# Kernel tuning notes

Measured on AMD Instinct MI355X. Metric: run time of the kernel, lower is better.

Reference implementation:

```python
import jax, jax.numpy as jnp
import numpy as np

N_NODES = 150000
N_EDGES = 2400000
N_GRAPHS = 1024
EPS = 1e-5


def setup_inputs() -> dict:
    key = jax.random.key(0)
    ks = jax.random.split(key, 20)
    x = jax.random.normal(ks[0], (N_NODES, 3), dtype=jnp.float32)
    edge_index = jax.random.randint(ks[1], (2, N_EDGES), 0, N_NODES, dtype=jnp.int64)
    batch = jnp.sort(jax.random.randint(ks[2], (N_NODES,), 0, N_GRAPHS, dtype=jnp.int64))

    def glorot(k, shape):
        fan_in, fan_out = shape[0], shape[1]
        lim = jnp.sqrt(6.0 / (fan_in + fan_out)).astype(jnp.float32)
        return jax.random.uniform(k, shape, jnp.float32, -lim, lim)

    params = dict(
        W1=glorot(ks[3], (3, 32)), b1=jnp.zeros((32,), jnp.float32),
        gn1_w=jnp.ones((32,), jnp.float32), gn1_b=jnp.zeros((32,), jnp.float32), gn1_ms=jnp.ones((32,), jnp.float32),
        W2=glorot(ks[4], (32, 32)), b2=jnp.zeros((32,), jnp.float32),
        gn2_w=jnp.ones((32,), jnp.float32), gn2_b=jnp.zeros((32,), jnp.float32), gn2_ms=jnp.ones((32,), jnp.float32),
        W3=glorot(ks[5], (32, 32)), b3=jnp.zeros((32,), jnp.float32),
        gn3_w=jnp.ones((32,), jnp.float32), gn3_b=jnp.zeros((32,), jnp.float32), gn3_ms=jnp.ones((32,), jnp.float32),
        lin_w=glorot(ks[6], (32, 3)), lin_b=jnp.zeros((3,), jnp.float32),
    )
    return dict(x=x, edge_index=edge_index, batch=batch, **params)


def _gcn_conv(x, W, b, src, dst, dinv_sqrt):
    # PyG GCNConv: h = x @ W; propagate with sym-normalized A + self-loops; + bias
    h = x @ W  # [N, F]
    coef = dinv_sqrt[src] * dinv_sqrt[dst]  # [E]
    msgs = h[src] * coef[:, None]  # [E, F]
    agg = jax.ops.segment_sum(msgs, dst, num_segments=N_NODES)
    agg = agg + (dinv_sqrt * dinv_sqrt)[:, None] * h  # self-loop term
    return agg + b


def _graph_norm(x, batch, counts, weight, bias, mean_scale):
    # PyG GraphNorm: per-graph mean/var with learnable mean_scale
    mean = jax.ops.segment_sum(x, batch, num_segments=N_GRAPHS) / counts[:, None]
    out = x - mean_scale * mean[batch]
    var = jax.ops.segment_sum(out * out, batch, num_segments=N_GRAPHS) / counts[:, None]
    std = jnp.sqrt(var + EPS)
    return weight * out / std[batch] + bias


def reference(x, edge_index, batch,
              W1, b1, gn1_w, gn1_b, gn1_ms,
              W2, b2, gn2_w, gn2_b, gn2_ms,
              W3, b3, gn3_w, gn3_b, gn3_ms,
              lin_w, lin_b):
    src, dst = edge_index[0], edge_index[1]
    # degree over A + I (edge weight 1)
    deg = jax.ops.segment_sum(jnp.ones((N_EDGES,), jnp.float32), dst, num_segments=N_NODES) + 1.0
    dinv_sqrt = jax.lax.rsqrt(deg)
    counts = jax.ops.segment_sum(jnp.ones((N_NODES,), jnp.float32), batch, num_segments=N_GRAPHS)

    x1 = jax.nn.relu(_graph_norm(_gcn_conv(x, W1, b1, src, dst, dinv_sqrt), batch, counts, gn1_w, gn1_b, gn1_ms))
    h2 = _graph_norm(_gcn_conv(x1, W2, b2, src, dst, dinv_sqrt), batch, counts, gn2_w, gn2_b, gn2_ms)
    x2 = jax.nn.relu(h2 + x1)
    h3 = _graph_norm(_gcn_conv(x2, W3, b3, src, dst, dinv_sqrt), batch, counts, gn3_w, gn3_b, gn3_ms)
    x3 = jax.nn.relu(h3 + x2)

    pooled = jax.ops.segment_sum(x3, batch, num_segments=N_GRAPHS) / counts[:, None]  # mean pool
    return pooled @ lin_w + lin_b  # [G, 3]
```

## Files before the change

kernel.cpp:

```cpp
#include <hip/hip_runtime.h>

#define N_NODES 150000
#define N_EDGES 2400000
#define N_GRAPHS 1024
#define F 32
#define EPSV 1e-5f

#define BS 256
#define NB ((N_NODES + BS - 1) / BS)
#define CAP 5120
#define EB 8192
#define NEB ((N_EDGES + EB - 1) / EB)
#define EPT (EB / 256)
#define KPT (CAP / 256)

__device__ __forceinline__ float bflo(unsigned int u) {
    union { unsigned int i; float f; } v; v.i = u << 16; return v.f;
}
__device__ __forceinline__ float bfhi(unsigned int u) {
    union { unsigned int i; float f; } v; v.i = u & 0xffff0000u; return v.f;
}
__device__ __forceinline__ unsigned int f2bf(float f) {
    union { float f; unsigned int i; } v; v.f = f;
    unsigned int r = v.i + 0x7fff + ((v.i >> 16) & 1);
    return r >> 16;
}

__global__ void k_init(const int* __restrict__ batch, int* __restrict__ bucketCur,
                       int* __restrict__ off, float* __restrict__ gstats) {
    int i = blockIdx.x * blockDim.x + threadIdx.x;
    if (i >= N_NODES) return;
    if (i < NB) bucketCur[i] = i * CAP;
    if (i < N_GRAPHS * 9) gstats[i] = 0.f;
    int b = batch[i];
    if (i == 0) {
        for (int g = 0; g <= b; ++g) off[g] = 0;
    } else {
        int pb = batch[i - 1];
        for (int g = pb + 1; g <= b; ++g) off[g] = i;
    }
    if (i == N_NODES - 1) {
        for (int g = b + 1; g <= N_GRAPHS; ++g) off[g] = N_NODES;
    }
}

__global__ __launch_bounds__(256) void k_bin(const int* __restrict__ src,
                                             const int* __restrict__ dst,
                                             int* __restrict__ bucketCur,
                                             unsigned int* __restrict__ binned) {
    __shared__ int h[NB];
    __shared__ int gb[NB];
    int t = threadIdx.x;
    for (int b = t; b < NB; b += 256) h[b] = 0;
    __syncthreads();
    int base = blockIdx.x * EB + t;
    unsigned int key[EPT];
    unsigned int pk[EPT];
#pragma unroll
    for (int k = 0; k < EPT; ++k) {
        int e = base + k * 256;
        if (e < N_EDGES) {
            int d = dst[e];
            int b = d >> 8;
            key[k] = ((unsigned int)(d & 255) << 18) | (unsigned int)src[e];
            unsigned int rk = (unsigned int)atomicAdd(&h[b], 1);
            pk[k] = (rk << 10) | (unsigned int)b;
        } else {
            pk[k] = 0xFFFFFFFFu;
        }
    }
    __syncthreads();
    for (int b = t; b < NB; b += 256) {
        int c = h[b];
        gb[b] = c ? atomicAdd(&bucketCur[b], c) : 0;
    }
    __syncthreads();
#pragma unroll
    for (int k = 0; k < EPT; ++k) {
        if (pk[k] != 0xFFFFFFFFu) {
            unsigned int b = pk[k] & 1023u;
            unsigned int rk = pk[k] >> 10;
            binned[gb[b] + rk] = key[k];
        }
    }
}

__global__ __launch_bounds__(256) void k_csr(const unsigned int* __restrict__ binned,
                                             const int* __restrict__ bucketCur,
                                             const float* __restrict__ x,
                                             unsigned int* __restrict__ rowptr,
                                             float* __restrict__ dinv,
                                             float* __restrict__ xs4,
                                             int* __restrict__ csr) {
    __shared__ int lcnt[256];
    __shared__ int lpre[256];
    __shared__ int sc[256];
    int b = blockIdx.x, t = threadIdx.x;
    int e0 = b * CAP;
    int e1 = bucketCur[b];
    lcnt[t] = 0;
    __syncthreads();
    unsigned int kc[KPT];
#pragma unroll
    for (int k = 0; k < KPT; ++k) {
        int e = e0 + t + k * 256;
        if (e < e1) {
            kc[k] = binned[e];
            atomicAdd(&lcnt[kc[k] >> 18], 1);
        }
    }
    __syncthreads();
    int v = lcnt[t];
    sc[t] = v;
    __syncthreads();
    for (int o = 1; o < 256; o <<= 1) {
        int x2 = (t >= o) ? sc[t - o] : 0;
        __syncthreads();
        sc[t] += x2;
        __syncthreads();
    }
    int excl = sc[t] - v;
    lpre[t] = excl;
    int gnode = b * BS + t;
    if (gnode < N_NODES) {
        rowptr[gnode] = ((unsigned int)(e0 + excl) << 8) | (unsigned int)min(v, 255);
        float dv = rsqrtf((float)v + 1.0f);
        dinv[gnode] = dv;
        float4 xv;
        xv.x = x[gnode * 3 + 0] * dv;
        xv.y = x[gnode * 3 + 1] * dv;
        xv.z = x[gnode * 3 + 2] * dv;
        xv.w = 0.f;
        ((float4*)xs4)[gnode] = xv;
    }
    lcnt[t] = 0;
    __syncthreads();
#pragma unroll
    for (int k = 0; k < KPT; ++k) {
        int e = e0 + t + k * 256;
        if (e < e1) {
            unsigned int key = kc[k];
            int ld = key >> 18;
            int pos = atomicAdd(&lcnt[ld], 1);
            csr[e0 + lpre[ld] + pos] = (int)(key & 0x3FFFFu);
        }
    }
}

__global__ __launch_bounds__(256) void k_gz(
        const float* __restrict__ xs4, const int* __restrict__ csr,
        const unsigned int* __restrict__ rowptr, const float* __restrict__ dinv,
        const int* __restrict__ batch,
        float* __restrict__ zs4, float* __restrict__ gstats) {
    __shared__ float st[8 * 12];
    __shared__ int gbase_s;
    int t = threadIdx.x;
    for (int i = t; i < 8 * 12; i += 256) st[i] = 0.f;
    if (t == 0) gbase_s = batch[blockIdx.x * 128];
    __syncthreads();

    int gid = blockIdx.x * 256 + t;
    int n = gid >> 1, h = gid & 1;
    float z0 = 0.f, z1 = 0.f, z2 = 0.f;
    if (n < N_NODES) {
        const float4* xv = (const float4*)xs4;
        unsigned int rp = rowptr[n];
        int st0 = (int)(rp >> 8);
        int len = (int)(rp & 255u);
        int half0 = (len + 1) >> 1;
        int e  = h ? (st0 + half0) : st0;
        int e1 = h ? (st0 + len)   : (st0 + half0);
        if (!h) {
            float4 sv = xv[n];
            z0 = sv.x; z1 = sv.y; z2 = sv.z;
        }
        for (; e + 3 < e1; e += 4) {
            int s0 = csr[e], s1 = csr[e + 1], s2 = csr[e + 2], s3 = csr[e + 3];
            float4 u0 = xv[s0], u1 = xv[s1], u2 = xv[s2], u3 = xv[s3];
            z0 += u0.x + u1.x + u2.x + u3.x;
            z1 += u0.y + u1.y + u2.y + u3.y;
            z2 += u0.z + u1.z + u2.z + u3.z;
        }
        for (; e < e1; ++e) {
            float4 u = xv[csr[e]];
            z0 += u.x; z1 += u.y; z2 += u.z;
        }
    }
    z0 += __shfl_down(z0, 1);
    z1 += __shfl_down(z1, 1);
    z2 += __shfl_down(z2, 1);
    if (h == 0 && n < N_NODES) {
        float dd = dinv[n];
        z0 *= dd; z1 *= dd; z2 *= dd;
        float4 zv; zv.x = z0; zv.y = z1; zv.z = z2; zv.w = 0.f;
        ((float4*)zs4)[n] = zv;
        int g = batch[n];
        int lg = g - gbase_s;
        if (lg < 8) {
            float* sp = &st[lg * 12];
            atomicAdd(&sp[0], z0);      atomicAdd(&sp[1], z1);
            atomicAdd(&sp[2], z2);      atomicAdd(&sp[3], z0 * z0);
            atomicAdd(&sp[4], z0 * z1); atomicAdd(&sp[5], z0 * z2);
            atomicAdd(&sp[6], z1 * z1); atomicAdd(&sp[7], z1 * z2);
            atomicAdd(&sp[8], z2 * z2);
        } else {
            float* gp = &gstats[g * 9];
            atomicAdd(&gp[0], z0);      atomicAdd(&gp[1], z1);
            atomicAdd(&gp[2], z2);      atomicAdd(&gp[3], z0 * z0);
            atomicAdd(&gp[4], z0 * z1); atomicAdd(&gp[5], z0 * z2);
            atomicAdd(&gp[6], z1 * z1); atomicAdd(&gp[7], z1 * z2);
            atomicAdd(&gp[8], z2 * z2);
        }
    }
    __syncthreads();
    if (t < 72) {
        int slot = t / 9, k = t % 9;
        int g = gbase_s + slot;
        float v = st[slot * 12 + k];
        if (g < N_GRAPHS && v != 0.f) atomicAdd(&gstats[g * 9 + k], v);
    }
}

__global__ __launch_bounds__(256) void k_prep(
        const float* __restrict__ gstats, const int* __restrict__ off,
        const float* __restrict__ W, const float* __restrict__ bias,
        const float* __restrict__ gw, const float* __restrict__ gms,
        float* __restrict__ mvA, float* __restrict__ scA) {
    int gid = blockIdx.x * 256 + threadIdx.x;
    if (gid >= N_GRAPHS * F) return;
    int g = gid >> 5, f = gid & 31;
    float rc = 1.0f / (float)(off[g + 1] - off[g]);
    const float* sp = &gstats[g * 9];
    float S0 = sp[0], S1 = sp[1], S2 = sp[2];
    float m00 = sp[3], m01 = sp[4], m02 = sp[5], m11 = sp[6], m12 = sp[7], m22 = sp[8];
    float w0 = W[0 * F + f], w1 = W[1 * F + f], w2 = W[2 * F + f];
    float b = bias[f];
    float sy = w0 * S0 + w1 * S1 + w2 * S2;
    float m = sy * rc + b;
    float q = w0 * w0 * m00 + w1 * w1 * m11 + w2 * w2 * m22
            + 2.f * (w0 * w1 * m01 + w0 * w2 * m02 + w1 * w2 * m12);
    float Ey2 = q * rc + 2.f * b * (sy * rc) + b * b;
    float mv = gms[f] * m;
    float var = Ey2 - 2.f * mv * m + mv * mv;
    mvA[gid] = mv;
    scA[gid] = gw[f] * rsqrtf(var + EPSV);
}

__global__ __launch_bounds__(256) void k_n1(
        const float* __restrict__ zs4, const int* __restrict__ batch,
        const float* __restrict__ dinv,
        const float* __restrict__ W, const float* __restrict__ bias,
        const float* __restrict__ gb,
        const float* __restrict__ mvA, const float* __restrict__ scA,
        unsigned short* __restrict__ xh, float* __restrict__ outp) {
    int gid = blockIdx.x * 256 + threadIdx.x;
    int n = gid >> 3, c = gid & 7;
    if (n >= N_NODES) return;
    float4 zv = ((const float4*)zs4)[n];
    float z0 = zv.x, z1 = zv.y, z2 = zv.z;
    int g = batch[n];
    float dd = dinv[n];
    float4 w0 = ((const float4*)(W + 0 * F))[c];
    float4 w1 = ((const float4*)(W + 1 * F))[c];
    float4 w2 = ((const float4*)(W + 2 * F))[c];
    float4 y  = ((const float4*)bias)[c];
    y.x += z0 * w0.x + z1 * w1.x + z2 * w2.x;
    y.y += z0 * w0.y + z1 * w1.y + z2 * w2.y;
    y.z += z0 * w0.z + z1 * w1.z + z2 * w2.z;
    y.w += z0 * w0.w + z1 * w1.w + z2 * w2.w;
    float4 mv = ((const float4*)mvA)[g * 8 + c];
    float4 sc = ((const float4*)scA)[g * 8 + c];
    float4 bb = ((const float4*)gb)[c];
    float4 o;
    o.x = fmaxf((y.x - mv.x) * sc.x + bb.x, 0.f);
    o.y = fmaxf((y.y - mv.y) * sc.y + bb.y, 0.f);
    o.z = fmaxf((y.z - mv.z) * sc.z + bb.z, 0.f);
    o.w = fmaxf((y.w - mv.w) * sc.w + bb.w, 0.f);
    ((float4*)outp)[n * 8 + c] = o;
    uint2 hp;
    hp.x = f2bf(o.x * dd) | (f2bf(o.y * dd) << 16);
    hp.y = f2bf(o.z * dd) | (f2bf(o.w * dd) << 16);
    ((uint2*)xh)[n * 8 + c] = hp;
}

__global__ __launch_bounds__(256) void k_gat32(
        const unsigned short* __restrict__ xh, const int* __restrict__ csr,
        const unsigned int* __restrict__ rowptr, const float* __restrict__ dinv,
        const float* __restrict__ W, const float* __restrict__ bias,
        float* __restrict__ y) {
    __shared__ float Ws[F * F];
    __shared__ float bs[F];
    __shared__ float Zs[64 * 36];
    int t = threadIdx.x;
    ((float4*)Ws)[t] = ((const float4*)W)[t];
    if (t < F) bs[t] = bias[t];
    __syncthreads();

    int gid = blockIdx.x * 256 + t;
    int n = gid >> 2, c = gid & 3, ln = t >> 2;
    bool act = (n < N_NODES);
    float acc[8];
    if (act) {
        const uint4* xr = (const uint4*)xh;
        uint4 us = xr[n * 4 + c];
        acc[0] = bflo(us.x); acc[1] = bfhi(us.x);
        acc[2] = bflo(us.y); acc[3] = bfhi(us.y);
        acc[4] = bflo(us.z); acc[5] = bfhi(us.z);
        acc[6] = bflo(us.w); acc[7] = bfhi(us.w);
        unsigned int rp = rowptr[n];
        int e = (int)(rp >> 8);
        int e1 = e + (int)(rp & 255u);
        for (; e + 3 < e1; e += 4) {
            int s0 = csr[e], s1 = csr[e + 1], s2 = csr[e + 2], s3 = csr[e + 3];
            uint4 u0 = xr[s0 * 4 + c];
            uint4 u1 = xr[s1 * 4 + c];
            uint4 u2 = xr[s2 * 4 + c];
            uint4 u3 = xr[s3 * 4 + c];
            acc[0] += bflo(u0.x); acc[1] += bfhi(u0.x);
            acc[2] += bflo(u0.y); acc[3] += bfhi(u0.y);
            acc[4] += bflo(u0.z); acc[5] += bfhi(u0.z);
            acc[6] += bflo(u0.w); acc[7] += bfhi(u0.w);
            acc[0] += bflo(u1.x); acc[1] += bfhi(u1.x);
            acc[2] += bflo(u1.y); acc[3] += bfhi(u1.y);
            acc[4] += bflo(u1.z); acc[5] += bfhi(u1.z);
            acc[6] += bflo(u1.w); acc[7] += bfhi(u1.w);
            acc[0] += bflo(u2.x); acc[1] += bfhi(u2.x);
            acc[2] += bflo(u2.y); acc[3] += bfhi(u2.y);
            acc[4] += bflo(u2.z); acc[5] += bfhi(u2.z);
            acc[6] += bflo(u2.w); acc[7] += bfhi(u2.w);
            acc[0] += bflo(u3.x); acc[1] += bfhi(u3.x);
            acc[2] += bflo(u3.y); acc[3] += bfhi(u3.y);
            acc[4] += bflo(u3.z); acc[5] += bfhi(u3.z);
            acc[6] += bflo(u3.w); acc[7] += bfhi(u3.w);
        }
        for (; e < e1; ++e) {
            int s0 = csr[e];
            uint4 u0 = xr[s0 * 4 + c];
            acc[0] += bflo(u0.x); acc[1] += bfhi(u0.x);
            acc[2] += bflo(u0.y); acc[3] += bfhi(u0.y);
            acc[4] += bflo(u0.z); acc[5] += bfhi(u0.z);
            acc[6] += bflo(u0.w); acc[7] += bfhi(u0.w);
        }
        float dd = dinv[n];
#pragma unroll
        for (int j = 0; j < 8; ++j) acc[j] *= dd;
    } else {
#pragma unroll
        for (int j = 0; j < 8; ++j) acc[j] = 0.f;
    }
    *(float4*)&Zs[ln * 36 + c * 8]     = *(float4*)&acc[0];
    *(float4*)&Zs[ln * 36 + c * 8 + 4] = *(float4*)&acc[4];
    __syncthreads();

    if (act) {
        const float* zrow = &Zs[ln * 36];
        float4 o0 = ((const float4*)bs)[c * 2];
        float4 o1 = ((const float4*)bs)[c * 2 + 1];
#pragma unroll
        for (int k = 0; k < F; ++k) {
            float zk = zrow[k];
            float4 w0 = ((const float4*)&Ws[k * F])[c * 2];
            float4 w1 = ((const float4*)&Ws[k * F])[c * 2 + 1];
            o0.x += zk * w0.x; o0.y += zk * w0.y; o0.z += zk * w0.z; o0.w += zk * w0.w;
            o1.x += zk * w1.x; o1.y += zk * w1.y; o1.z += zk * w1.z; o1.w += zk * w1.w;
        }
        ((float4*)y)[n * 8 + c * 2]     = o0;
        ((float4*)y)[n * 8 + c * 2 + 1] = o1;
    }
}

template <bool RES, bool WXH>
__global__ __launch_bounds__(256) void k_gn2(
        const float* agg, const float* res, const int* __restrict__ off,
        const float* __restrict__ gw, const float* __restrict__ gb,
        const float* __restrict__ gms, const float* __restrict__ dinv,
        unsigned short* __restrict__ xh, float* outp) {
    __shared__ float red1[256], red2[256];
    __shared__ float mv_s[F], sc_s[F];
    int g = blockIdx.x;
    int i0 = off[g], i1 = off[g + 1];
    float rc = 1.0f / (float)(i1 - i0);
    int t = threadIdx.x;
    int f = t & 31, r0 = t >> 5;

    float s = 0.f, q = 0.f;
    for (int n = i0 + r0; n < i1; n += 8) {
        float v = agg[n * F + f];
        s += v; q += v * v;
    }
    red1[t] = s; red2[t] = q; __syncthreads();
    if (t < 128) { red1[t] += red1[t + 128]; red2[t] += red2[t + 128]; } __syncthreads();
    if (t < 64)  { red1[t] += red1[t + 64];  red2[t] += red2[t + 64];  } __syncthreads();
    if (t < 32) {
        float sm = (red1[t] + red1[t + 32]) * rc;
        float sq = (red2[t] + red2[t + 32]) * rc;
        float mv = gms[t] * sm;
        float var = sq - mv * (2.f * sm - mv);
        mv_s[t] = mv;
        sc_s[t] = gw[t] * rsqrtf(var + EPSV);
    }
    __syncthreads();

    float w = sc_s[f], mv = mv_s[f], bb = gb[f];
    for (int n = i0 + r0; n < i1; n += 8) {
        float y = (agg[n * F + f] - mv) * w + bb;
        if (RES) y += res[n * F + f];
        y = fmaxf(y, 0.f);
        outp[n * F + f] = y;
        if (WXH) xh[n * F + f] = (unsigned short)f2bf(y * dinv[n]);
    }
}

__global__ __launch_bounds__(256) void k_gnfin(
        const float* __restrict__ agg, const float* __restrict__ res,
        const int* __restrict__ off,
        const float* __restrict__ gw, const float* __restrict__ gb,
        const float* __restrict__ gms,
        const float* __restrict__ lin_w, const float* __restrict__ lin_b,
        float* __restrict__ outp) {
    __shared__ float red1[256], red2[256];
    __shared__ float mv_s[F], sc_s[F], pooled_s[F];
    int g = blockIdx.x;
    int i0 = off[g], i1 = off[g + 1];
    float cnt = (float)(i1 - i0);
    float rc = 1.0f / cnt;
    int t = threadIdx.x;
    int f = t & 31, r0 = t >> 5;

    float s = 0.f, q = 0.f;
    for (int n = i0 + r0; n < i1; n += 8) {
        float v = agg[n * F + f];
        s += v; q += v * v;
    }
    red1[t] = s; red2[t] = q; __syncthreads();
    if (t < 128) { red1[t] += red1[t + 128]; red2[t] += red2[t + 128]; } __syncthreads();
    if (t < 64)  { red1[t] += red1[t + 64];  red2[t] += red2[t + 64];  } __syncthreads();
    if (t < 32) {
        float sm = (red1[t] + red1[t + 32]) * rc;
        float sq = (red2[t] + red2[t + 32]) * rc;
        float mv = gms[t] * sm;
        float var = sq - mv * (2.f * sm - mv);
        mv_s[t] = mv;
        sc_s[t] = gw[t] * rsqrtf(var + EPSV);
    }
    __syncthreads();

    float w = sc_s[f], mv = mv_s[f], bb = gb[f];
    float ps = 0.f;
    for (int n = i0 + r0; n < i1; n += 8) {
        float yv = (agg[n * F + f] - mv) * w + bb + res[n * F + f];
        ps += fmaxf(yv, 0.f);
    }
    __syncthreads();
    red1[t] = ps; __syncthreads();
    if (t < 128) red1[t] += red1[t + 128]; __syncthreads();
    if (t < 64)  red1[t] += red1[t + 64];  __syncthreads();
    if (t < 32) { red1[t] += red1[t + 32]; pooled_s[t] = red1[t] * rc; }
    __syncthreads();
    if (t < 3) {
        float o = lin_b[t];
#pragma unroll
        for (int f2 = 0; f2 < F; ++f2) o += pooled_s[f2] * lin_w[f2 * 3 + t];
        outp[g * 3 + t] = o;
    }
}

extern "C" void kernel_launch(void* const* d_in, const int* in_sizes, int n_in,
                              void* d_out, int out_size, void* d_ws, size_t ws_size,
                              hipStream_t stream) {
    const float* x      = (const float*)d_in[0];
    const int*   ei     = (const int*)d_in[1];
    const int*   batch  = (const int*)d_in[2];
    const float* W1     = (const float*)d_in[3];
    const float* b1     = (const float*)d_in[4];
    const float* gn1w   = (const float*)d_in[5];
    const float* gn1b   = (const float*)d_in[6];
    const float* gn1ms  = (const float*)d_in[7];
    const float* W2     = (const float*)d_in[8];
    const float* b2     = (const float*)d_in[9];
    const float* gn2w   = (const float*)d_in[10];
    const float* gn2b   = (const float*)d_in[11];
    const float* gn2ms  = (const float*)d_in[12];
    const float* W3     = (const float*)d_in[13];
    const float* b3     = (const float*)d_in[14];
    const float* gn3w   = (const float*)d_in[15];
    const float* gn3b   = (const float*)d_in[16];
    const float* gn3ms  = (const float*)d_in[17];
    const float* lin_w  = (const float*)d_in[18];
    const float* lin_b  = (const float*)d_in[19];
    float* out = (float*)d_out;

    const int* srcp = ei;
    const int* dstp = ei + N_EDGES;

    char* ws = (char*)d_ws;
    size_t p = 0;
    auto alloc = [&](size_t bytes) {
        size_t r = p; p += (bytes + 511) & ~(size_t)511; return r;
    };
    int*   off       = (int*)  (ws + alloc(sizeof(int) * (N_GRAPHS + 1)));
    int*   bucketCur = (int*)  (ws + alloc(sizeof(int) * NB));
    unsigned int* rowptr = (unsigned int*)(ws + alloc(sizeof(unsigned int) * N_NODES));
    float* dinv      = (float*)(ws + alloc(sizeof(float) * N_NODES));
    float* xs4       = (float*)(ws + alloc(sizeof(float) * N_NODES * 4));
    float* zs4       = (float*)(ws + alloc(sizeof(float) * N_NODES * 4));
    float* gstats    = (float*)(ws + alloc(sizeof(float) * N_GRAPHS * 9));
    float* mvA       = (float*)(ws + alloc(sizeof(float) * N_GRAPHS * F));
    float* scA       = (float*)(ws + alloc(sizeof(float) * N_GRAPHS * F));
    unsigned int* binned = (unsigned int*)(ws + alloc(sizeof(unsigned int) * NB * CAP));
    int*   csr       = (int*)  (ws + alloc(sizeof(int) * NB * CAP));
    float* A         = (float*)(ws + alloc(sizeof(float) * N_NODES * F));
    float* B         = (float*)(ws + alloc(sizeof(float) * N_NODES * F));
    unsigned short* xh = (unsigned short*)binned;
    (void)ws_size; (void)n_in; (void)in_sizes; (void)out_size;

    const int TB = 256;
    dim3 blk(TB);
    int ngrid  = (N_NODES + TB - 1) / TB;
    int ggrid2 = (N_NODES * 2 + TB - 1) / TB;
    int ggrid8 = (N_NODES * 8 + TB - 1) / TB;
    int ggrid4 = (N_NODES * 4 + TB - 1) / TB;

    k_init<<<ngrid, blk, 0, stream>>>(batch, bucketCur, off, gstats);
    k_bin <<<NEB, blk, 0, stream>>>(srcp, dstp, bucketCur, binned);
    k_csr <<<NB, blk, 0, stream>>>(binned, bucketCur, x, rowptr, dinv, xs4, csr);

    k_gz  <<<ggrid2, blk, 0, stream>>>(xs4, csr, rowptr, dinv, batch, zs4, gstats);
    k_prep<<<(N_GRAPHS * F + TB - 1) / TB, blk, 0, stream>>>(
        gstats, off, W1, b1, gn1w, gn1ms, mvA, scA);
    k_n1  <<<ggrid8, blk, 0, stream>>>(zs4, batch, dinv, W1, b1, gn1b, mvA, scA, xh, A);

    k_gat32<<<ggrid4, blk, 0, stream>>>(xh, csr, rowptr, dinv, W2, b2, B);
    k_gn2<true, true><<<N_GRAPHS, blk, 0, stream>>>(
        B, A, off, gn2w, gn2b, gn2ms, dinv, xh, B);

    k_gat32<<<ggrid4, blk, 0, stream>>>(xh, csr, rowptr, dinv, W3, b3, A);
    k_gnfin<<<N_GRAPHS, blk, 0, stream>>>(A, B, off, gn3w, gn3b, gn3ms,
                                          lin_w, lin_b, out);
}
```

Measured before the change: 305.8 us.

## Reorder nodes by in-degree within each bucket to balance gather wavefronts

k_csr now builds a per-256-node-block permutation that counts-sorts nodes by in-degree and writes it to a porder array. The gather kernels k_gz and k_gat32 read node ids through this permutation, so lanes in the same wavefront walk neighbour lists of similar length. This is meant to cut divergence and idle lanes in the edge loops. The cost is an extra indirection load per node, a second shared-memory scan in k_csr, and less coalesced per-node stores and batch reads, which also breaks the contiguous-graph assumption in the k_gz stats path.

```diff
diff --git a/kernel.cpp b/kernel.cpp
--- a/kernel.cpp
+++ b/kernel.cpp
@@ -8,6 +8,7 @@
 
 #define BS 256
 #define NB ((N_NODES + BS - 1) / BS)
+#define NPAD (NB * BS)
 #define CAP 5120
 #define EB 8192
 #define NEB ((N_EDGES + EB - 1) / EB)
@@ -91,14 +92,17 @@
                                              unsigned int* __restrict__ rowptr,
                                              float* __restrict__ dinv,
                                              float* __restrict__ xs4,
-                                             int* __restrict__ csr) {
+                                             int* __restrict__ csr,
+                                             int* __restrict__ porder) {
     __shared__ int lcnt[256];
     __shared__ int lpre[256];
     __shared__ int sc[256];
+    __shared__ int dhist[256];
     int b = blockIdx.x, t = threadIdx.x;
     int e0 = b * CAP;
     int e1 = bucketCur[b];
     lcnt[t] = 0;
+    dhist[t] = 0;
     __syncthreads();
     unsigned int kc[KPT];
 #pragma unroll
@@ -122,8 +126,9 @@
     int excl = sc[t] - v;
     lpre[t] = excl;
     int gnode = b * BS + t;
+    int dv8 = min(v, 255);
     if (gnode < N_NODES) {
-        rowptr[gnode] = ((unsigned int)(e0 + excl) << 8) | (unsigned int)min(v, 255);
+        rowptr[gnode] = ((unsigned int)(e0 + excl) << 8) | (unsigned int)dv8;
         float dv = rsqrtf((float)v + 1.0f);
         dinv[gnode] = dv;
         float4 xv;
@@ -132,8 +137,27 @@
         xv.z = x[gnode * 3 + 2] * dv;
         xv.w = 0.f;
         ((float4*)xs4)[gnode] = xv;
-    }
+    } else {
+        dv8 = 0;
+    }
+    atomicAdd(&dhist[dv8], 1);
     lcnt[t] = 0;
+    __syncthreads();
+    int dvv = dhist[t];
+    sc[t] = dvv;
+    __syncthreads();
+    for (int o = 1; o < 256; o <<= 1) {
+        int x2 = (t >= o) ? sc[t - o] : 0;
+        __syncthreads();
+        sc[t] += x2;
+        __syncthreads();
+    }
+    dhist[t] = sc[t] - dvv;
+    __syncthreads();
+    {
+        int pos = atomicAdd(&dhist[dv8], 1);
+        porder[b * BS + pos] = gnode;
+    }
     __syncthreads();
 #pragma unroll
     for (int k = 0; k < KPT; ++k) {
@@ -150,17 +174,18 @@
 __global__ __launch_bounds__(256) void k_gz(
         const float* __restrict__ xs4, const int* __restrict__ csr,
         const unsigned int* __restrict__ rowptr, const float* __restrict__ dinv,
-        const int* __restrict__ batch,
+        const int* __restrict__ batch, const int* __restrict__ porder,
         float* __restrict__ zs4, float* __restrict__ gstats) {
     __shared__ float st[8 * 12];
     __shared__ int gbase_s;
     int t = threadIdx.x;
     for (int i = t; i < 8 * 12; i += 256) st[i] = 0.f;
-    if (t == 0) gbase_s = batch[blockIdx.x * 128];
+    if (t == 0) gbase_s = batch[min((int)(blockIdx.x >> 1) * BS, N_NODES - 1)];
     __syncthreads();
 
     int gid = blockIdx.x * 256 + t;
-    int n = gid >> 1, h = gid & 1;
+    int slot = gid >> 1, h = gid & 1;
+    int n = (slot < NPAD) ? porder[slot] : N_NODES;
     float z0 = 0.f, z1 = 0.f, z2 = 0.f;
     if (n < N_NODES) {
         const float4* xv = (const float4*)xs4;
@@ -196,7 +221,7 @@
         ((float4*)zs4)[n] = zv;
         int g = batch[n];
         int lg = g - gbase_s;
-        if (lg < 8) {
+        if (lg >= 0 && lg < 8) {
             float* sp = &st[lg * 12];
             atomicAdd(&sp[0], z0);      atomicAdd(&sp[1], z1);
             atomicAdd(&sp[2], z2);      atomicAdd(&sp[3], z0 * z0);
@@ -214,9 +239,9 @@
     }
     __syncthreads();
     if (t < 72) {
-        int slot = t / 9, k = t % 9;
-        int g = gbase_s + slot;
-        float v = st[slot * 12 + k];
+        int slot2 = t / 9, k = t % 9;
+        int g = gbase_s + slot2;
+        float v = st[slot2 * 12 + k];
         if (g < N_GRAPHS && v != 0.f) atomicAdd(&gstats[g * 9 + k], v);
     }
 }
@@ -286,6 +311,7 @@
 __global__ __launch_bounds__(256) void k_gat32(
         const unsigned short* __restrict__ xh, const int* __restrict__ csr,
         const unsigned int* __restrict__ rowptr, const float* __restrict__ dinv,
+        const int* __restrict__ porder,
         const float* __restrict__ W, const float* __restrict__ bias,
         float* __restrict__ y) {
     __shared__ float Ws[F * F];
@@ -297,7 +323,8 @@
     __syncthreads();
 
     int gid = blockIdx.x * 256 + t;
-    int n = gid >> 2, c = gid & 3, ln = t >> 2;
+    int slot = gid >> 2, c = gid & 3, ln = t >> 2;
+    int n = (slot < NPAD) ? porder[slot] : N_NODES;
     bool act = (n < N_NODES);
     float acc[8];
     if (act) {
@@ -507,6 +534,7 @@
     float* gstats    = (float*)(ws + alloc(sizeof(float) * N_GRAPHS * 9));
     float* mvA       = (float*)(ws + alloc(sizeof(float) * N_GRAPHS * F));
     float* scA       = (float*)(ws + alloc(sizeof(float) * N_GRAPHS * F));
+    int*   porder    = (int*)  (ws + alloc(sizeof(int) * NPAD));
     unsigned int* binned = (unsigned int*)(ws + alloc(sizeof(unsigned int) * NB * CAP));
     int*   csr       = (int*)  (ws + alloc(sizeof(int) * NB * CAP));
     float* A         = (float*)(ws + alloc(sizeof(float) * N_NODES * F));
@@ -517,24 +545,24 @@
     const int TB = 256;
     dim3 blk(TB);
     int ngrid  = (N_NODES + TB - 1) / TB;
-    int ggrid2 = (N_NODES * 2 + TB - 1) / TB;
+    int ggrid2 = (NPAD * 2 + TB - 1) / TB;
     int ggrid8 = (N_NODES * 8 + TB - 1) / TB;
-    int ggrid4 = (N_NODES * 4 + TB - 1) / TB;
+    int ggrid4 = (NPAD * 4 + TB - 1) / TB;
 
     k_init<<<ngrid, blk, 0, stream>>>(batch, bucketCur, off, gstats);
     k_bin <<<NEB, blk, 0, stream>>>(srcp, dstp, bucketCur, binned);
-    k_csr <<<NB, blk, 0, stream>>>(binned, bucketCur, x, rowptr, dinv, xs4, csr);
-
-    k_gz  <<<ggrid2, blk, 0, stream>>>(xs4, csr, rowptr, dinv, batch, zs4, gstats);
+    k_csr <<<NB, blk, 0, stream>>>(binned, bucketCur, x, rowptr, dinv, xs4, csr, porder);
+
+    k_gz  <<<ggrid2, blk, 0, stream>>>(xs4, csr, rowptr, dinv, batch, porder, zs4, gstats);
     k_prep<<<(N_GRAPHS * F + TB - 1) / TB, blk, 0, stream>>>(
         gstats, off, W1, b1, gn1w, gn1ms, mvA, scA);
     k_n1  <<<ggrid8, blk, 0, stream>>>(zs4, batch, dinv, W1, b1, gn1b, mvA, scA, xh, A);
 
-    k_gat32<<<ggrid4, blk, 0, stream>>>(xh, csr, rowptr, dinv, W2, b2, B);
+    k_gat32<<<ggrid4, blk, 0, stream>>>(xh, csr, rowptr, dinv, porder, W2, b2, B);
     k_gn2<true, true><<<N_GRAPHS, blk, 0, stream>>>(
         B, A, off, gn2w, gn2b, gn2ms, dinv, xh, B);
 
-    k_gat32<<<ggrid4, blk, 0, stream>>>(xh, csr, rowptr, dinv, W3, b3, A);
+    k_gat32<<<ggrid4, blk, 0, stream>>>(xh, csr, rowptr, dinv, porder, W3, b3, A);
     k_gnfin<<<N_GRAPHS, blk, 0, stream>>>(A, B, off, gn3w, gn3b, gn3ms,
                                           lin_w, lin_b, out);
 }
```

After: 328.6 us. 7.4% more time.
